# Optimization experiments

Hardware: AMD Instinct MI355X
Metric: run time of the kernel (lower is better)

The kernel has to match this reference:

```python
import jax, jax.numpy as jnp
import numpy as np

DIMS = [64, 32, 12, 8, 6, 2]


def setup_inputs() -> dict:
    key = jax.random.key(0)
    ks = jax.random.split(key, 1 + 2 * (len(DIMS) - 1))
    inp = {"x": jax.random.normal(ks[0], (1048576, DIMS[0]), dtype=jnp.float32)}
    for i in range(len(DIMS) - 1):
        fan_in = DIMS[i]
        bound = 1.0 / np.sqrt(fan_in)
        inp[f"W{i}"] = jax.random.uniform(ks[1 + 2 * i], (DIMS[i], DIMS[i + 1]), jnp.float32, -bound, bound)
        inp[f"b{i}"] = jax.random.uniform(ks[2 + 2 * i], (DIMS[i + 1],), jnp.float32, -bound, bound)
    return inp


def reference(x, W0, b0, W1, b1, W2, b2, W3, b3, W4, b4):
    # 5-layer Linear+ReLU chain (final layer has no ReLU), matching nn.Sequential.
    h = jax.nn.relu(x @ W0 + b0)
    h = jax.nn.relu(h @ W1 + b1)
    h = jax.nn.relu(h @ W2 + b2)
    h = jax.nn.relu(h @ W3 + b3)
    return h @ W4 + b4  # [B, 2]
```

## Files before the change

### kernel.cpp

```cpp
#include <hip/hip_runtime.h>


typedef __attribute__((ext_vector_type(8))) short short8;
typedef __attribute__((ext_vector_type(16))) float f32x16;
typedef __attribute__((ext_vector_type(4))) unsigned uint4v;
typedef __attribute__((address_space(3))) void* as3p;
typedef const __attribute__((address_space(1))) void* as1p;

#define BLOCK 64
#define NT 4
#define BUFSZ 8576

__device__ __forceinline__ unsigned fbits(float x) {
    return __builtin_bit_cast(unsigned, x);
}
__device__ __forceinline__ float asf(unsigned u) {
    return __builtin_bit_cast(float, u);
}
__device__ __forceinline__ unsigned packhi(unsigned ua, unsigned ub) {
    return __builtin_amdgcn_perm(ub, ua, 0x07060302u);
}
__device__ __forceinline__ short8 mk_hi(const float* f) {
    uint4v w;
#pragma unroll
    for (int t = 0; t < 4; ++t)
        w[t] = packhi(fbits(f[2 * t]), fbits(f[2 * t + 1]));
    return __builtin_bit_cast(short8, w);
}
__device__ __forceinline__ short8 mk_lo(const float* f) {
    uint4v w;
#pragma unroll
    for (int t = 0; t < 4; ++t) {
        const float la = f[2 * t]     - asf(fbits(f[2 * t])     & 0xFFFF0000u);
        const float lb = f[2 * t + 1] - asf(fbits(f[2 * t + 1]) & 0xFFFF0000u);
        w[t] = packhi(fbits(la), fbits(lb));
    }
    return __builtin_bit_cast(short8, w);
}
#define MFMA(A, B, C) __builtin_amdgcn_mfma_f32_32x32x16_bf16(A, B, C, 0, 0, 0)

template <int IN, int OUT, bool RELU>
__device__ __forceinline__ void layer(const float* __restrict__ W,
                                      const float* __restrict__ b,
                                      const float* h_in, float* h_out) {
#pragma unroll
    for (int o = 0; o < OUT; ++o) h_out[o] = b[o];
#pragma unroll
    for (int i = 0; i < IN; ++i) {
        const float v = h_in[i];
#pragma unroll
        for (int o = 0; o < OUT; ++o)
            h_out[o] = fmaf(v, W[i * OUT + o], h_out[o]);
    }
    if (RELU) {
#pragma unroll
        for (int o = 0; o < OUT; ++o) h_out[o] = fmaxf(h_out[o], 0.0f);
    }
}

__global__ __launch_bounds__(BLOCK, 3) void mlp_kernel(
        const float* __restrict__ x,
        const float* __restrict__ W0, const float* __restrict__ b0,
        const float* __restrict__ W1, const float* __restrict__ b1,
        const float* __restrict__ W2, const float* __restrict__ b2,
        const float* __restrict__ W3, const float* __restrict__ b3,
        const float* __restrict__ W4, const float* __restrict__ b4,
        float* __restrict__ out, int nrows) {
    extern __shared__ char lds[];
    char* const bA = lds;
    char* const bB = lds + BUFSZ;

    const int lane = threadIdx.x;
    const long long row0 = (long long)blockIdx.x * (NT * 64);
    const char* xbase = reinterpret_cast<const char*>(x + row0 * 64);

    const int r0 = lane & 31;
    const int hA = lane >> 5;
    const int rb = r0 * 256 + (r0 >> 2) * 48 + hA * 32;

    const int colB = lane & 31;
    short8 W0h_, W0l_, W1h_, W1l_, W2h_, W2l_, W3h_, W3l_;
    {
        float wf[8];
#define LOADB(s, BH, BL)                                                \
        {                                                               \
            _Pragma("unroll")                                           \
            for (int j = 0; j < 8; ++j)                                 \
                wf[j] = W0[((s) * 16 + 8 * hA + j) * 32 + colB];        \
            BH = mk_hi(wf);                                             \
            BL = mk_lo(wf);                                             \
        }
        LOADB(0, W0h_, W0l_)
        LOADB(1, W1h_, W1l_)
        LOADB(2, W2h_, W2l_)
        LOADB(3, W3h_, W3l_)
#undef LOADB
    }

    auto STAGEH = [&](int g, char* buf) {
        const char* s0 = xbase + g * 8192 + lane * 16;
#pragma unroll
        for (int k = 0; k < 8; ++k)
            __builtin_amdgcn_global_load_lds((as1p)(s0 + k * 1024),
                                             (as3p)(buf + k * 1072), 16, 0, 0);
    };

    STAGEH(0, bA);

#pragma unroll 1
    for (int tt = 0; tt < NT; ++tt) {
        f32x16 accA, accB;
#pragma unroll
        for (int r = 0; r < 16; ++r) { accA[r] = 0.0f; accB[r] = 0.0f; }

#define KSTEP(CUR, s, WH, WL, ACC)                                         \
        {                                                                  \
            float f[8];                                                    \
            const float4 q0 = *reinterpret_cast<const float4*>(            \
                (CUR) + rb + (s) * 64);                                    \
            const float4 q1 = *reinterpret_cast<const float4*>(            \
                (CUR) + rb + (s) * 64 + 16);                               \
            f[0]=q0.x; f[1]=q0.y; f[2]=q0.z; f[3]=q0.w;                    \
            f[4]=q1.x; f[5]=q1.y; f[6]=q1.z; f[7]=q1.w;                    \
            const short8 Xh = mk_hi(f), Xl = mk_lo(f);                     \
            ACC = MFMA(WH, Xh, ACC);                                       \
            ACC = MFMA(WL, Xh, ACC);                                       \
            ACC = MFMA(WH, Xl, ACC);                                       \
        }

        {
            STAGEH(2 * tt + 1, bB);
            asm volatile("s_waitcnt vmcnt(8)" ::: "memory");
            __builtin_amdgcn_sched_barrier(0);
            KSTEP(bA, 0, W0h_, W0l_, accA)
            KSTEP(bA, 1, W1h_, W1l_, accA)
            KSTEP(bA, 2, W2h_, W2l_, accA)
            KSTEP(bA, 3, W3h_, W3l_, accA)
        }
        {
            if (tt + 1 < NT) {
                STAGEH(2 * tt + 2, bA);
                asm volatile("s_waitcnt vmcnt(8)" ::: "memory");
            } else {
                asm volatile("s_waitcnt vmcnt(0)" ::: "memory");
            }
            __builtin_amdgcn_sched_barrier(0);
            KSTEP(bB, 0, W0h_, W0l_, accB)
            KSTEP(bB, 1, W1h_, W1l_, accB)
            KSTEP(bB, 2, W2h_, W2l_, accB)
            KSTEP(bB, 3, W3h_, W3l_, accB)
        }
#undef KSTEP

        float xr[32];
#pragma unroll
        for (int reg = 0; reg < 16; ++reg) {
            float a = accA[reg];
            float b = accB[reg];
            asm("v_permlane32_swap_b32 %0, %1" : "+v"(a), "+v"(b));
            const int f0 = (reg & 3) + 8 * (reg >> 2);
            xr[f0]     = fmaxf(a + b0[f0],     0.0f);
            xr[f0 + 4] = fmaxf(b + b0[f0 + 4], 0.0f);
        }

        float h1[12], h2[8], h3[6], h4[2];
        layer<32, 12, true>(W1, b1, xr, h1);
        layer<12, 8, true>(W2, b2, h1, h2);
        layer<8, 6, true>(W3, b3, h2, h3);
        layer<6, 2, false>(W4, b4, h3, h4);

        reinterpret_cast<float2*>(out)[row0 + tt * 64 + lane] =
            make_float2(h4[0], h4[1]);
    }
}

extern "C" void kernel_launch(void* const* d_in, const int* in_sizes, int n_in,
                              void* d_out, int out_size, void* d_ws, size_t ws_size,
                              hipStream_t stream) {
    const float* x  = (const float*)d_in[0];
    const float* W0 = (const float*)d_in[1];
    const float* b0 = (const float*)d_in[2];
    const float* W1 = (const float*)d_in[3];
    const float* b1 = (const float*)d_in[4];
    const float* W2 = (const float*)d_in[5];
    const float* b2 = (const float*)d_in[6];
    const float* W3 = (const float*)d_in[7];
    const float* b3 = (const float*)d_in[8];
    const float* W4 = (const float*)d_in[9];
    const float* b4 = (const float*)d_in[10];
    float* out = (float*)d_out;

    const int nrows = in_sizes[0] / 64;
    const int rows_per_block = NT * 64;
    const int grid = nrows / rows_per_block;
    const size_t shmem = 2 * BUFSZ;

    mlp_kernel<<<grid, BLOCK, shmem, stream>>>(x, W0, b0, W1, b1, W2, b2,
                                               W3, b3, W4, b4, out, nrows);
}
```

Before: 66.47 us.

## Replace LDS-staged x loads with direct register loads and 4-wave blocks

Drops the global_load_lds staging into shared memory and instead loads each lane's x fragments straight from global memory into registers, double-buffered across two register sets. The block grows from one wave to four, and each wave handles 8 tiles instead of 4, so the grid shrinks. This removes the LDS round trip and the manual vmcnt waits, at the cost of more register pressure, less coalesced strided global reads, and fewer blocks in flight.

Result: faster. 55.91 us (-15.9%).

```diff
diff --git a/kernel.cpp b/kernel.cpp
--- a/kernel.cpp
+++ b/kernel.cpp
@@ -4,12 +4,9 @@
 typedef __attribute__((ext_vector_type(8))) short short8;
 typedef __attribute__((ext_vector_type(16))) float f32x16;
 typedef __attribute__((ext_vector_type(4))) unsigned uint4v;
-typedef __attribute__((address_space(3))) void* as3p;
-typedef const __attribute__((address_space(1))) void* as1p;
 
-#define BLOCK 64
-#define NT 4
-#define BUFSZ 8576
+#define BLOCK 256
+#define NT 8
 
 __device__ __forceinline__ unsigned fbits(float x) {
     return __builtin_bit_cast(unsigned, x);
@@ -58,7 +55,7 @@
     }
 }
 
-__global__ __launch_bounds__(BLOCK, 3) void mlp_kernel(
+__global__ __launch_bounds__(BLOCK, 2) void mlp_kernel(
         const float* __restrict__ x,
         const float* __restrict__ W0, const float* __restrict__ b0,
         const float* __restrict__ W1, const float* __restrict__ b1,
@@ -66,23 +63,21 @@
         const float* __restrict__ W3, const float* __restrict__ b3,
         const float* __restrict__ W4, const float* __restrict__ b4,
         float* __restrict__ out, int nrows) {
-    extern __shared__ char lds[];
-    char* const bA = lds;
-    char* const bB = lds + BUFSZ;
+    const int t = threadIdx.x;
+    const int wv = t >> 6;
+    const int lane = t & 63;
 
-    const int lane = threadIdx.x;
-    const long long row0 = (long long)blockIdx.x * (NT * 64);
-    const char* xbase = reinterpret_cast<const char*>(x + row0 * 64);
+    const long long row0 = ((long long)blockIdx.x * 4 + wv) * (NT * 64);
+    const char* hbase = reinterpret_cast<const char*>(x + row0 * 64) +
+                        (lane & 31) * 256 + (lane >> 5) * 32;
 
-    const int r0 = lane & 31;
     const int hA = lane >> 5;
-    const int rb = r0 * 256 + (r0 >> 2) * 48 + hA * 32;
+    const int colB = lane & 31;
 
-    const int colB = lane & 31;
     short8 W0h_, W0l_, W1h_, W1l_, W2h_, W2l_, W3h_, W3l_;
     {
         float wf[8];
-#define LOADB(s, BH, BL)                                                \
+#define LOADW(s, BH, BL)                                                \
         {                                                               \
             _Pragma("unroll")                                           \
             for (int j = 0; j < 8; ++j)                                 \
@@ -90,67 +85,61 @@
             BH = mk_hi(wf);                                             \
             BL = mk_lo(wf);                                             \
         }
-        LOADB(0, W0h_, W0l_)
-        LOADB(1, W1h_, W1l_)
-        LOADB(2, W2h_, W2l_)
-        LOADB(3, W3h_, W3l_)
-#undef LOADB
+        LOADW(0, W0h_, W0l_)
+        LOADW(1, W1h_, W1l_)
+        LOADW(2, W2h_, W2l_)
+        LOADW(3, W3h_, W3l_)
+#undef LOADW
     }
 
-    auto STAGEH = [&](int g, char* buf) {
-        const char* s0 = xbase + g * 8192 + lane * 16;
-#pragma unroll
-        for (int k = 0; k < 8; ++k)
-            __builtin_amdgcn_global_load_lds((as1p)(s0 + k * 1024),
-                                             (as3p)(buf + k * 1072), 16, 0, 0);
-    };
+    float4 A0, A1, A2, A3, A4, A5, A6, A7;
+    float4 B0, B1, B2, B3, B4, B5, B6, B7;
 
-    STAGEH(0, bA);
+#define LOADH(OFF, P)                                                      \
+    P##0 = *reinterpret_cast<const float4*>(hbase + (OFF) + 0);            \
+    P##1 = *reinterpret_cast<const float4*>(hbase + (OFF) + 16);           \
+    P##2 = *reinterpret_cast<const float4*>(hbase + (OFF) + 64);           \
+    P##3 = *reinterpret_cast<const float4*>(hbase + (OFF) + 80);           \
+    P##4 = *reinterpret_cast<const float4*>(hbase + (OFF) + 128);          \
+    P##5 = *reinterpret_cast<const float4*>(hbase + (OFF) + 144);          \
+    P##6 = *reinterpret_cast<const float4*>(hbase + (OFF) + 192);          \
+    P##7 = *reinterpret_cast<const float4*>(hbase + (OFF) + 208);          \
+    __builtin_amdgcn_sched_barrier(0);
+
+#define KSTEP(Q0, Q1, WH, WL, ACC)                                         \
+    {                                                                      \
+        float f[8];                                                        \
+        f[0] = Q0.x; f[1] = Q0.y; f[2] = Q0.z; f[3] = Q0.w;                \
+        f[4] = Q1.x; f[5] = Q1.y; f[6] = Q1.z; f[7] = Q1.w;                \
+        const short8 Xh = mk_hi(f), Xl = mk_lo(f);                         \
+        ACC = MFMA(WH, Xh, ACC);                                           \
+        ACC = MFMA(WL, Xh, ACC);                                           \
+        ACC = MFMA(WH, Xl, ACC);                                           \
+    }
+
+    LOADH(0, A)
 
 #pragma unroll 1
     for (int tt = 0; tt < NT; ++tt) {
+        const long long toff = (long long)tt * 16384;
+
         f32x16 accA, accB;
 #pragma unroll
         for (int r = 0; r < 16; ++r) { accA[r] = 0.0f; accB[r] = 0.0f; }
 
-#define KSTEP(CUR, s, WH, WL, ACC)                                         \
-        {                                                                  \
-            float f[8];                                                    \
-            const float4 q0 = *reinterpret_cast<const float4*>(            \
-                (CUR) + rb + (s) * 64);                                    \
-            const float4 q1 = *reinterpret_cast<const float4*>(            \
-                (CUR) + rb + (s) * 64 + 16);                               \
-            f[0]=q0.x; f[1]=q0.y; f[2]=q0.z; f[3]=q0.w;                    \
-            f[4]=q1.x; f[5]=q1.y; f[6]=q1.z; f[7]=q1.w;                    \
-            const short8 Xh = mk_hi(f), Xl = mk_lo(f);                     \
-            ACC = MFMA(WH, Xh, ACC);                                       \
-            ACC = MFMA(WL, Xh, ACC);                                       \
-            ACC = MFMA(WH, Xl, ACC);                                       \
+        LOADH(toff + 8192, B)
+        KSTEP(A0, A1, W0h_, W0l_, accA)
+        KSTEP(A2, A3, W1h_, W1l_, accA)
+        KSTEP(A4, A5, W2h_, W2l_, accA)
+        KSTEP(A6, A7, W3h_, W3l_, accA)
+
+        if (tt + 1 < NT) {
+            LOADH(toff + 16384, A)
         }
-
-        {
-            STAGEH(2 * tt + 1, bB);
-            asm volatile("s_waitcnt vmcnt(8)" ::: "memory");
-            __builtin_amdgcn_sched_barrier(0);
-            KSTEP(bA, 0, W0h_, W0l_, accA)
-            KSTEP(bA, 1, W1h_, W1l_, accA)
-            KSTEP(bA, 2, W2h_, W2l_, accA)
-            KSTEP(bA, 3, W3h_, W3l_, accA)
-        }
-        {
-            if (tt + 1 < NT) {
-                STAGEH(2 * tt + 2, bA);
-                asm volatile("s_waitcnt vmcnt(8)" ::: "memory");
-            } else {
-                asm volatile("s_waitcnt vmcnt(0)" ::: "memory");
-            }
-            __builtin_amdgcn_sched_barrier(0);
-            KSTEP(bB, 0, W0h_, W0l_, accB)
-            KSTEP(bB, 1, W1h_, W1l_, accB)
-            KSTEP(bB, 2, W2h_, W2l_, accB)
-            KSTEP(bB, 3, W3h_, W3l_, accB)
-        }
-#undef KSTEP
+        KSTEP(B0, B1, W0h_, W0l_, accB)
+        KSTEP(B2, B3, W1h_, W1l_, accB)
+        KSTEP(B4, B5, W2h_, W2l_, accB)
+        KSTEP(B6, B7, W3h_, W3l_, accB)
 
         float xr[32];
 #pragma unroll
@@ -172,6 +161,8 @@
         reinterpret_cast<float2*>(out)[row0 + tt * 64 + lane] =
             make_float2(h4[0], h4[1]);
     }
+#undef LOADH
+#undef KSTEP
 }
 
 extern "C" void kernel_launch(void* const* d_in, const int* in_sizes, int n_in,
@@ -191,10 +182,9 @@
     float* out = (float*)d_out;
 
     const int nrows = in_sizes[0] / 64;
-    const int rows_per_block = NT * 64;
+    const int rows_per_block = 4 * NT * 64;
     const int grid = nrows / rows_per_block;
-    const size_t shmem = 2 * BUFSZ;
 
-    mlp_kernel<<<grid, BLOCK, shmem, stream>>>(x, W0, b0, W1, b1, W2, b2,
-                                               W3, b3, W4, b4, out, nrows);
+    mlp_kernel<<<grid, BLOCK, 0, stream>>>(x, W0, b0, W1, b1, W2, b2,
+                                           W3, b3, W4, b4, out, nrows);
 }
```
